# Kernel tuning notes

Hardware: AMD Instinct MI355X
Metric: run time of the kernel (lower is better)

## Reference

```python
import jax, jax.numpy as jnp
import numpy as np

B, S, D, H = 2, 4096, 1024, 16
HD = D // H  # 64


def setup_inputs() -> dict:
    key = jax.random.key(0)
    ks = jax.random.split(key, 6)
    return {
        "x": jax.random.normal(ks[0], (B, S, D), dtype=jnp.float32),
        "mask": jax.random.normal(ks[1], (B, S, S), dtype=jnp.float32),
        "Wqkv": jax.random.normal(ks[2], (D, 3 * D), dtype=jnp.float32) * 0.02,
        "bqkv": jax.random.normal(ks[3], (3 * D,), dtype=jnp.float32) * 0.02,
        "Wo": jax.random.normal(ks[4], (D, D), dtype=jnp.float32) * 0.02,
        "bo": jax.random.normal(ks[5], (D,), dtype=jnp.float32) * 0.02,
    }


def reference(x, mask, Wqkv, bqkv, Wo, bo):
    b, s, d = x.shape
    # fused QKV projection: [B,S,3D]
    qkv = jnp.einsum('bsd,de->bse', x, Wqkv) + bqkv
    # [B,S,H,3*HD] -> [B,H,S,3*HD]
    qkv = qkv.reshape(b, s, H, 3 * HD).transpose(0, 2, 1, 3)
    q, k, v = jnp.split(qkv, 3, axis=-1)  # each [B,H,S,HD]
    scale = 1.0 / jnp.sqrt(jnp.asarray(HD, dtype=x.dtype))
    scores = jnp.einsum('bhqe,bhke->bhqk', q, k) * scale  # [B,H,S,S]
    scores = scores + mask[:, None, :, :]  # additive mask broadcast over heads
    attn = jax.nn.softmax(scores, axis=-1)
    values = jnp.einsum('bhqk,bhke->bhqe', attn, v)  # [B,H,S,HD]
    # NOTE: faithful to original TF code: reshape WITHOUT transposing heads back
    values = values.reshape(b, s, d)
    out = jnp.einsum('bsd,de->bse', values, Wo) + bo
    return out
```

## Files before the change

### kernel.cpp

```cpp
#include <hip/hip_runtime.h>
#include <hip/hip_bf16.h>

#define DEV __device__ __forceinline__

typedef unsigned short u16;
typedef __attribute__((ext_vector_type(4))) float f32x4;
typedef __attribute__((ext_vector_type(8))) short s16x8;

static constexpr int Bc = 2, Hc = 16, Sc = 4096, Dc = 1024, HDc = 64;

DEV u16 f2bf(float f) {
  unsigned x = __float_as_uint(f);
  x += 0x7FFFu + ((x >> 16) & 1u);
  return (u16)(x >> 16);
}
DEV float bf2f(u16 u) { return __uint_as_float(((unsigned)u) << 16); }

DEV unsigned cvtpk_bf16(float lo, float hi) {
  unsigned r;
  asm("v_cvt_pk_bf16_f32 %0, %1, %2" : "=v"(r) : "v"(lo), "v"(hi));
  return r;
}

DEV void gload_lds16(const void* g, void* l) {
  __builtin_amdgcn_global_load_lds((const __attribute__((address_space(1))) void*)g,
                                   (__attribute__((address_space(3))) void*)l, 16, 0, 0);
}

DEV f32x4 mfma16(s16x8 a, s16x8 b, f32x4 c) {
  return __builtin_amdgcn_mfma_f32_16x16x32_bf16(a, b, c, 0, 0, 0);
}

DEV f32x4 fzero4() { f32x4 v; v[0] = v[1] = v[2] = v[3] = 0.f; return v; }

__global__ void cvt_f32_bf16(const float* __restrict__ in, u16* __restrict__ out, size_t n) {
  size_t i = ((size_t)blockIdx.x * blockDim.x + threadIdx.x) * 4;
  size_t stride = (size_t)gridDim.x * blockDim.x * 4;
  for (; i < n; i += stride) {
    float4 v = *(const float4*)(in + i);
    u16 a = f2bf(v.x), b = f2bf(v.y), c = f2bf(v.z), d = f2bf(v.w);
    *(ushort4*)(out + i) = make_ushort4(a, b, c, d);
  }
}

__global__ void transpose_cvt(const float* __restrict__ in, u16* __restrict__ out, int R, int C) {
  __shared__ u16 t[64][72];
  int nct = C >> 6;
  int tr = blockIdx.x / nct, tc = blockIdx.x % nct;
  int r0 = tr << 6, c0 = tc << 6;
  int lr = threadIdx.x >> 2;
  int lc0 = (threadIdx.x & 3) << 4;
  const float* src = in + (size_t)(r0 + lr) * C + c0 + lc0;
#pragma unroll
  for (int j = 0; j < 16; j += 4) {
    float4 v = *(const float4*)(src + j);
    t[lr][lc0 + j + 0] = f2bf(v.x);
    t[lr][lc0 + j + 1] = f2bf(v.y);
    t[lr][lc0 + j + 2] = f2bf(v.z);
    t[lr][lc0 + j + 3] = f2bf(v.w);
  }
  __syncthreads();
  u16* dst = out + (size_t)(c0 + lr) * R + r0 + lc0;
#pragma unroll
  for (int j = 0; j < 16; j += 4) {
    u16 a = t[lc0 + j + 0][lr], b = t[lc0 + j + 1][lr], c = t[lc0 + j + 2][lr], d = t[lc0 + j + 3][lr];
    *(ushort4*)(dst + j) = make_ushort4(a, b, c, d);
  }
}

template <int MODE>
__global__ __launch_bounds__(256, 2) void gemm128(
    const u16* __restrict__ A, const u16* __restrict__ BT, const float* __restrict__ bias,
    void* __restrict__ out0, u16* __restrict__ out1, u16* __restrict__ out2,
    int N, int K, int grid_n) {
  __shared__ u16 Al[128 * 64];
  __shared__ u16 Bl[128 * 64];
  int bid = blockIdx.x;
  int bn = bid % grid_n, bm = bid / grid_n;
  int m0 = bm * 128, n0 = bn * 128;
  int tid = threadIdx.x, lane = tid & 63, wid = tid >> 6;
  int wm = wid >> 1, wn = wid & 1;
  int fr = lane & 15, fg = lane >> 4;

  f32x4 acc[4][4];
#pragma unroll
  for (int mi = 0; mi < 4; ++mi)
#pragma unroll
    for (int ni = 0; ni < 4; ++ni) acc[mi][ni] = fzero4();

  for (int kt = 0; kt < K; kt += 64) {
    const u16* Ag = A + (size_t)m0 * K + kt;
    const u16* Bg = BT + (size_t)n0 * K + kt;
#pragma unroll
    for (int it = 0; it < 4; ++it) {
      int L = it * 4096 + wid * 1024 + lane * 16;
      int row = L >> 7;
      int sch = ((L >> 4) & 7) ^ (row & 7);
      gload_lds16(Ag + (size_t)row * K + sch * 8, (char*)Al + it * 4096 + wid * 1024);
      gload_lds16(Bg + (size_t)row * K + sch * 8, (char*)Bl + it * 4096 + wid * 1024);
    }
    __syncthreads();
#pragma unroll
    for (int c = 0; c < 2; ++c) {
      s16x8 af[4], bfr[4];
#pragma unroll
      for (int mi = 0; mi < 4; ++mi) {
        int row = wm * 64 + mi * 16 + fr;
        int ch = (c * 4 + fg) ^ (row & 7);
        af[mi] = *(const s16x8*)((const char*)Al + row * 128 + ch * 16);
      }
#pragma unroll
      for (int ni = 0; ni < 4; ++ni) {
        int row = wn * 64 + ni * 16 + fr;
        int ch = (c * 4 + fg) ^ (row & 7);
        bfr[ni] = *(const s16x8*)((const char*)Bl + row * 128 + ch * 16);
      }
#pragma unroll
      for (int mi = 0; mi < 4; ++mi)
#pragma unroll
        for (int ni = 0; ni < 4; ++ni) acc[mi][ni] = mfma16(af[mi], bfr[ni], acc[mi][ni]);
    }
    __syncthreads();
  }

  if constexpr (MODE == 0) {
    u16* qb = (u16*)out0;
    u16* kb = out1;
    u16* vT = out2;
#pragma unroll
    for (int ni = 0; ni < 4; ++ni) {
      int n = n0 + wn * 64 + ni * 16 + fr;
      float bv = bias[n];
      int h = n / 192;
      int c = n % 192;
      int part = c >> 6;
      int e = c & 63;
#pragma unroll
      for (int mi = 0; mi < 4; ++mi) {
        int m = m0 + wm * 64 + mi * 16 + fg * 4;
        int b = m >> 12;
        int s = m & 4095;
        size_t bh = (size_t)b * Hc + h;
        if (part == 2) {
          u16 a0 = f2bf(acc[mi][ni][0] + bv), a1 = f2bf(acc[mi][ni][1] + bv);
          u16 a2 = f2bf(acc[mi][ni][2] + bv), a3 = f2bf(acc[mi][ni][3] + bv);
          *(ushort4*)(vT + ((bh * HDc + e) * (size_t)Sc + s)) = make_ushort4(a0, a1, a2, a3);
        } else {
          u16* dst = (part == 0 ? qb : kb) + ((bh * Sc + s) * (size_t)HDc + e);
#pragma unroll
          for (int r = 0; r < 4; ++r) dst[(size_t)r * HDc] = f2bf(acc[mi][ni][r] + bv);
        }
      }
    }
  } else {
    float* O = (float*)out0;
#pragma unroll
    for (int ni = 0; ni < 4; ++ni) {
      int n = n0 + wn * 64 + ni * 16 + fr;
      float bv = bias[n];
#pragma unroll
      for (int mi = 0; mi < 4; ++mi) {
        int m = m0 + wm * 64 + mi * 16 + fg * 4;
#pragma unroll
        for (int r = 0; r < 4; ++r) O[(size_t)(m + r) * N + n] = acc[mi][ni][r] + bv;
      }
    }
  }
}

template <int MB>
__global__ __launch_bounds__(512, 6) void attn_kernel(
    const u16* __restrict__ qb, const u16* __restrict__ kb, const u16* __restrict__ vT,
    const void* __restrict__ maskp, u16* __restrict__ vals) {
  __shared__ u16 Kl[64 * 64];
  __shared__ u16 Vl[64 * 64];
  __shared__ char Pl[8 * 16 * 144];

  int bid = ((blockIdx.x & 7) << 7) | (blockIdx.x >> 3);
  int h = bid & 15, b = (bid >> 4) & 1, qt = bid >> 5;
  int tid = threadIdx.x;
  int lane = tid & 63, wid = tid >> 6;
  int fr = lane & 15, fg = lane >> 4;
  size_t bh = (size_t)b * Hc + h;
  int q0 = qt * 128;
  int q = q0 + wid * 16 + fr;

  const u16* Qrow = qb + ((bh * Sc) + q) * (size_t)HDc;
  s16x8 qa0 = *(const s16x8*)(Qrow + fg * 8);
  s16x8 qa1 = *(const s16x8*)(Qrow + 32 + fg * 8);

  f32x4 o[4];
#pragma unroll
  for (int ef = 0; ef < 4; ++ef) o[ef] = fzero4();
  float mrun = -1e30f, lrun = 0.f;

  const u16* Kg = kb + bh * (size_t)Sc * HDc;
  const u16* Vg = vT + bh * (size_t)HDc * Sc;
  char* pw = (char*)Pl + wid * 2304 + fr * 144;
  const float SCALE = 0.125f;
  const float LOG2E = 1.44269504088896340736f;

  int srow = wid * 8 + (lane >> 3);
  int sch = (lane & 7) ^ (srow & 7);
  const u16* KgS = Kg + (size_t)srow * HDc + sch * 8;
  const u16* VgS = Vg + (size_t)srow * Sc + sch * 8;
  char* KlD = (char*)Kl + wid * 1024;
  char* VlD = (char*)Vl + wid * 1024;

  int kroff0 = fr * 128 + ((fg ^ (fr & 7)) << 4);
  int kroff1 = fr * 128 + (((4 + fg) ^ (fr & 7)) << 4);

  const u16* mk_b = (const u16*)maskp + ((size_t)b * Sc + q) * Sc + fg * 4;
  const float* mk_f = (const float*)maskp + ((size_t)b * Sc + q) * Sc + fg * 4;

  for (int kt = 0; kt < Sc / 64; ++kt) {
    gload_lds16(KgS + (size_t)kt * 4096, KlD);
    gload_lds16(VgS + (size_t)kt * 64, VlD);

    ushort4 m4[4];
    float4 mf[4];
    if (MB) {
#pragma unroll
      for (int f = 0; f < 4; ++f) m4[f] = *(const ushort4*)(mk_b + kt * 64 + f * 16);
    } else {
#pragma unroll
      for (int f = 0; f < 4; ++f) mf[f] = *(const float4*)(mk_f + kt * 64 + f * 16);
    }
    __syncthreads();

    f32x4 sa[4];
#pragma unroll
    for (int f = 0; f < 4; ++f) sa[f] = fzero4();
    __builtin_amdgcn_s_setprio(1);
#pragma unroll
    for (int f = 0; f < 4; ++f) {
      s16x8 kf = *(const s16x8*)((const char*)Kl + f * 2048 + kroff0);
      sa[f] = mfma16(kf, qa0, sa[f]);
    }
#pragma unroll
    for (int f = 0; f < 4; ++f) {
      s16x8 kf = *(const s16x8*)((const char*)Kl + f * 2048 + kroff1);
      sa[f] = mfma16(kf, qa1, sa[f]);
    }
    __builtin_amdgcn_s_setprio(0);

    float t[4][4];
#pragma unroll
    for (int f = 0; f < 4; ++f) {
      if (MB) {
        t[f][0] = fmaf(sa[f][0], SCALE, bf2f(m4[f].x));
        t[f][1] = fmaf(sa[f][1], SCALE, bf2f(m4[f].y));
        t[f][2] = fmaf(sa[f][2], SCALE, bf2f(m4[f].z));
        t[f][3] = fmaf(sa[f][3], SCALE, bf2f(m4[f].w));
      } else {
        t[f][0] = fmaf(sa[f][0], SCALE, mf[f].x);
        t[f][1] = fmaf(sa[f][1], SCALE, mf[f].y);
        t[f][2] = fmaf(sa[f][2], SCALE, mf[f].z);
        t[f][3] = fmaf(sa[f][3], SCALE, mf[f].w);
      }
    }

    float x0 = fmaxf(fmaxf(t[0][0], t[0][1]), t[0][2]);
    float x1 = fmaxf(fmaxf(t[0][3], t[1][0]), t[1][1]);
    float x2 = fmaxf(fmaxf(t[1][2], t[1][3]), t[2][0]);
    float x3 = fmaxf(fmaxf(t[2][1], t[2][2]), t[2][3]);
    float x4 = fmaxf(fmaxf(t[3][0], t[3][1]), t[3][2]);
    float mt = fmaxf(fmaxf(fmaxf(x0, x1), x2), fmaxf(fmaxf(x3, x4), t[3][3]));
    mt = fmaxf(mt, __shfl_xor(mt, 16, 64));
    mt = fmaxf(mt, __shfl_xor(mt, 32, 64));

    if (!__all(mt <= mrun + 8.0f)) {
      float mnew = fmaxf(mrun, mt);
      float al = __builtin_amdgcn_exp2f((mrun - mnew) * LOG2E);
      mrun = mnew;
      lrun *= al;
#pragma unroll
      for (int ef = 0; ef < 4; ++ef) o[ef] *= al;
    }

    float nm = -mrun * LOG2E;
    float p[4][4];
    float ss0 = 0.f, ss1 = 0.f;
#pragma unroll
    for (int f = 0; f < 4; ++f) {
      float p0 = __builtin_amdgcn_exp2f(fmaf(t[f][0], LOG2E, nm));
      float p1 = __builtin_amdgcn_exp2f(fmaf(t[f][1], LOG2E, nm));
      float p2 = __builtin_amdgcn_exp2f(fmaf(t[f][2], LOG2E, nm));
      float p3 = __builtin_amdgcn_exp2f(fmaf(t[f][3], LOG2E, nm));
      p[f][0] = p0; p[f][1] = p1; p[f][2] = p2; p[f][3] = p3;
      ss0 += (p0 + p1);
      ss1 += (p2 + p3);
    }
    float ssum = ss0 + ss1;
    ssum += __shfl_xor(ssum, 16, 64);
    ssum += __shfl_xor(ssum, 32, 64);
    lrun += ssum;

#pragma unroll
    for (int f = 0; f < 4; ++f) {
      uint2 pk;
      pk.x = cvtpk_bf16(p[f][0], p[f][1]);
      pk.y = cvtpk_bf16(p[f][2], p[f][3]);
      *(uint2*)(pw + f * 32 + fg * 8) = pk;
    }

    s16x8 pa0 = *(const s16x8*)(pw + fg * 16);
    s16x8 pa1 = *(const s16x8*)(pw + 64 + fg * 16);
    __builtin_amdgcn_s_setprio(1);
#pragma unroll
    for (int ef = 0; ef < 4; ++ef) {
      s16x8 vf = *(const s16x8*)((const char*)Vl + ef * 2048 + kroff0);
      o[ef] = mfma16(vf, pa0, o[ef]);
    }
#pragma unroll
    for (int ef = 0; ef < 4; ++ef) {
      s16x8 vf = *(const s16x8*)((const char*)Vl + ef * 2048 + kroff1);
      o[ef] = mfma16(vf, pa1, o[ef]);
    }
    __builtin_amdgcn_s_setprio(0);

    __syncthreads();
  }

  float inv = 1.f / lrun;
  u16* vbase = vals + (size_t)b * Sc * Dc + (size_t)h * Sc * HDc + (size_t)q * HDc;
#pragma unroll
  for (int ef = 0; ef < 4; ++ef) {
    ushort4 ov = make_ushort4(f2bf(o[ef][0] * inv), f2bf(o[ef][1] * inv),
                              f2bf(o[ef][2] * inv), f2bf(o[ef][3] * inv));
    *(ushort4*)(vbase + ef * 16 + fg * 4) = ov;
  }
}

extern "C" void kernel_launch(void* const* d_in, const int* in_sizes, int n_in,
                              void* d_out, int out_size, void* d_ws, size_t ws_size,
                              hipStream_t stream) {
  (void)in_sizes; (void)n_in; (void)out_size;
  const float* x    = (const float*)d_in[0];
  const float* mask = (const float*)d_in[1];
  const float* Wqkv = (const float*)d_in[2];
  const float* bqkv = (const float*)d_in[3];
  const float* Wo   = (const float*)d_in[4];
  const float* bo   = (const float*)d_in[5];
  float* out = (float*)d_out;
  char* ws = (char*)d_ws;

  u16* xb    = (u16*)(ws + 0);
  u16* wqkvT = (u16*)(ws + 16777216);
  u16* woT   = (u16*)(ws + 23068672);
  u16* qb    = (u16*)(ws + 25165824);
  u16* kb    = (u16*)(ws + 41943040);
  u16* vT    = (u16*)(ws + 58720256);
  u16* vals  = (u16*)(ws + 75497472);
  u16* maskb = (u16*)(ws + 92274688);
  int use_mb = (ws_size >= 159383552ull) ? 1 : 0;

  cvt_f32_bf16<<<dim3(2048), dim3(256), 0, stream>>>(x, xb, (size_t)8388608);
  if (use_mb)
    cvt_f32_bf16<<<dim3(4096), dim3(256), 0, stream>>>(mask, maskb, (size_t)33554432);
  transpose_cvt<<<dim3(768), dim3(256), 0, stream>>>(Wqkv, wqkvT, 1024, 3072);
  transpose_cvt<<<dim3(256), dim3(256), 0, stream>>>(Wo, woT, 1024, 1024);

  gemm128<0><<<dim3(1536), dim3(256), 0, stream>>>(xb, wqkvT, bqkv, (void*)qb, kb, vT,
                                                   3072, 1024, 24);
  if (use_mb)
    attn_kernel<1><<<dim3(1024), dim3(512), 0, stream>>>(qb, kb, vT, (const void*)maskb, vals);
  else
    attn_kernel<0><<<dim3(1024), dim3(512), 0, stream>>>(qb, kb, vT, (const void*)mask, vals);
  gemm128<1><<<dim3(512), dim3(256), 0, stream>>>(vals, woT, bo, (void*)out, nullptr, nullptr,
                                                  1024, 1024, 8);
}
```

Before: 497.5 us.

## Shrink attention blocks to 4 waves and prefetch next K/V tile during compute

The attention kernel drops from 8 to 4 waves per block (64 query rows), which doubles the grid to 2048 blocks. Each thread now stages two 16-byte chunks per K/V tile. K and V loads are also software-pipelined: the next K tile is issued right after the QK^T MFMAs and the next V tile after the PV MFMAs, so global-to-LDS transfer overlaps the softmax and the other matmul instead of stalling at the top of each iteration. The cost is that each block reloads K/V for fewer queries, which raises total K/V traffic, and it relies on the barrier placement to keep single-buffered LDS tiles from being overwritten while still in use.

```diff
diff --git a/kernel.cpp b/kernel.cpp
--- a/kernel.cpp
+++ b/kernel.cpp
@@ -169,20 +169,20 @@
 }
 
 template <int MB>
-__global__ __launch_bounds__(512, 6) void attn_kernel(
+__global__ __launch_bounds__(256, 6) void attn_kernel(
     const u16* __restrict__ qb, const u16* __restrict__ kb, const u16* __restrict__ vT,
     const void* __restrict__ maskp, u16* __restrict__ vals) {
   __shared__ u16 Kl[64 * 64];
   __shared__ u16 Vl[64 * 64];
-  __shared__ char Pl[8 * 16 * 144];
-
-  int bid = ((blockIdx.x & 7) << 7) | (blockIdx.x >> 3);
+  __shared__ char Pl[4 * 16 * 144];
+
+  int bid = ((blockIdx.x & 7) << 8) | (blockIdx.x >> 3);
   int h = bid & 15, b = (bid >> 4) & 1, qt = bid >> 5;
   int tid = threadIdx.x;
   int lane = tid & 63, wid = tid >> 6;
   int fr = lane & 15, fg = lane >> 4;
   size_t bh = (size_t)b * Hc + h;
-  int q0 = qt * 128;
+  int q0 = qt * 64;
   int q = q0 + wid * 16 + fr;
 
   const u16* Qrow = qb + ((bh * Sc) + q) * (size_t)HDc;
@@ -200,12 +200,17 @@
   const float SCALE = 0.125f;
   const float LOG2E = 1.44269504088896340736f;
 
-  int srow = wid * 8 + (lane >> 3);
-  int sch = (lane & 7) ^ (srow & 7);
-  const u16* KgS = Kg + (size_t)srow * HDc + sch * 8;
-  const u16* VgS = Vg + (size_t)srow * Sc + sch * 8;
-  char* KlD = (char*)Kl + wid * 1024;
-  char* VlD = (char*)Vl + wid * 1024;
+  int L0 = wid * 1024 + lane * 16;
+  int L1 = L0 + 4096;
+  int row0 = L0 >> 7, row1 = L1 >> 7;
+  int sch0 = ((L0 >> 4) & 7) ^ (row0 & 7);
+  int sch1 = ((L1 >> 4) & 7) ^ (row1 & 7);
+  const u16* KgS0 = Kg + (size_t)row0 * HDc + sch0 * 8;
+  const u16* KgS1 = Kg + (size_t)row1 * HDc + sch1 * 8;
+  const u16* VgS0 = Vg + (size_t)row0 * Sc + sch0 * 8;
+  const u16* VgS1 = Vg + (size_t)row1 * Sc + sch1 * 8;
+  char* KlD0 = (char*)Kl + L0;  char* KlD1 = (char*)Kl + L1;
+  char* VlD0 = (char*)Vl + L0;  char* VlD1 = (char*)Vl + L1;
 
   int kroff0 = fr * 128 + ((fg ^ (fr & 7)) << 4);
   int kroff1 = fr * 128 + (((4 + fg) ^ (fr & 7)) << 4);
@@ -213,10 +218,15 @@
   const u16* mk_b = (const u16*)maskp + ((size_t)b * Sc + q) * Sc + fg * 4;
   const float* mk_f = (const float*)maskp + ((size_t)b * Sc + q) * Sc + fg * 4;
 
-  for (int kt = 0; kt < Sc / 64; ++kt) {
-    gload_lds16(KgS + (size_t)kt * 4096, KlD);
-    gload_lds16(VgS + (size_t)kt * 64, VlD);
-
+  constexpr int NT = Sc / 64;
+
+  gload_lds16(KgS0, KlD0);
+  gload_lds16(KgS1, KlD1);
+  gload_lds16(VgS0, VlD0);
+  gload_lds16(VgS1, VlD1);
+  __syncthreads();
+
+  for (int kt = 0; kt < NT; ++kt) {
     ushort4 m4[4];
     float4 mf[4];
     if (MB) {
@@ -226,7 +236,6 @@
 #pragma unroll
       for (int f = 0; f < 4; ++f) mf[f] = *(const float4*)(mk_f + kt * 64 + f * 16);
     }
-    __syncthreads();
 
     f32x4 sa[4];
 #pragma unroll
@@ -243,6 +252,13 @@
       sa[f] = mfma16(kf, qa1, sa[f]);
     }
     __builtin_amdgcn_s_setprio(0);
+
+    __syncthreads();
+
+    if (kt + 1 < NT) {
+      gload_lds16(KgS0 + (size_t)(kt + 1) * 4096, KlD0);
+      gload_lds16(KgS1 + (size_t)(kt + 1) * 4096, KlD1);
+    }
 
     float t[4][4];
 #pragma unroll
@@ -320,6 +336,11 @@
     __builtin_amdgcn_s_setprio(0);
 
     __syncthreads();
+
+    if (kt + 1 < NT) {
+      gload_lds16(VgS0 + (size_t)(kt + 1) * 64, VlD0);
+      gload_lds16(VgS1 + (size_t)(kt + 1) * 64, VlD1);
+    }
   }
 
   float inv = 1.f / lrun;
@@ -364,9 +385,9 @@
   gemm128<0><<<dim3(1536), dim3(256), 0, stream>>>(xb, wqkvT, bqkv, (void*)qb, kb, vT,
                                                    3072, 1024, 24);
   if (use_mb)
-    attn_kernel<1><<<dim3(1024), dim3(512), 0, stream>>>(qb, kb, vT, (const void*)maskb, vals);
+    attn_kernel<1><<<dim3(2048), dim3(256), 0, stream>>>(qb, kb, vT, (const void*)maskb, vals);
   else
-    attn_kernel<0><<<dim3(1024), dim3(512), 0, stream>>>(qb, kb, vT, (const void*)mask, vals);
+    attn_kernel<0><<<dim3(2048), dim3(256), 0, stream>>>(qb, kb, vT, (const void*)mask, vals);
   gemm128<1><<<dim3(512), dim3(256), 0, stream>>>(vals, woT, bo, (void*)out, nullptr, nullptr,
                                                   1024, 1024, 8);
 }
```

Measured after the change: 479.2 us. 1.04x faster.
